# Kernel optimization log

Measured on AMD Instinct MI355X. Metric: run time of the kernel, lower is better.

Reference implementation:

```python
import jax, jax.numpy as jnp
import numpy as np

N = 10000      # atoms
E = 100000     # edges
C = 64         # hidden channels
S = 16         # spherical harmonic components (l_max=3)
NB = 8         # Bessel basis size
HID = 64       # radial MLP hidden
NE = 10        # chemical elements
G = 64         # graphs in batch
L = 2          # interaction layers
HEADS = 1
RC = 5.0       # radial cutoff
AVG_NEI = 16.0


def _sph_l3(u):
    # real spherical harmonics up to l=3, component normalization, on unit vectors u [E,3]
    x, y, z = u[..., 0], u[..., 1], u[..., 2]
    s3 = 3.0 ** 0.5; s5 = 5.0 ** 0.5; s15 = 15.0 ** 0.5
    c1 = (35.0 / 8.0) ** 0.5; c2 = 105.0 ** 0.5; c3 = (21.0 / 8.0) ** 0.5
    c4 = (7.0 / 4.0) ** 0.5; c5 = (105.0 / 4.0) ** 0.5
    comps = [jnp.ones_like(x),
             s3 * x, s3 * y, s3 * z,
             s15 * x * y, s15 * y * z, (s5 / 2) * (3 * z * z - 1), s15 * x * z, (s15 / 2) * (x * x - y * y),
             c1 * y * (3 * x * x - y * y), c2 * x * y * z, c3 * y * (5 * z * z - 1), c4 * z * (5 * z * z - 3),
             c3 * x * (5 * z * z - 1), c5 * z * (x * x - y * y), c1 * x * (x * x - 3 * y * y)]
    return jnp.stack(comps, axis=-1)  # [E, 16]


def _radial(r):
    # Bessel radial basis * polynomial cutoff (p=6); r [E,1] -> [E, NB]
    n = jnp.arange(1, NB + 1, dtype=r.dtype)
    bessel = (2.0 / RC) ** 0.5 * jnp.sin(n * jnp.pi * r / RC) / r
    t = r / RC
    p = 6.0
    fcut = 1.0 - (p + 1) * (p + 2) / 2 * t ** p + p * (p + 2) * t ** (p + 1) - p * (p + 1) / 2 * t ** (p + 2)
    fcut = jnp.where(r < RC, fcut, 0.0)
    return bessel * fcut


def setup_inputs() -> dict:
    key = jax.random.key(0)
    ks = jax.random.split(key, 20)
    positions = jax.random.uniform(ks[0], (N, 3), dtype=jnp.float32) * 6.0
    species = jax.random.randint(ks[1], (N,), 0, NE)
    node_attrs = jax.nn.one_hot(species, NE, dtype=jnp.float32)
    sender = jax.random.randint(ks[2], (E,), 0, N)
    offs = jax.random.randint(ks[3], (E,), 1, N)
    receiver = (sender + offs) % N  # no self loops
    edge_index = jnp.stack([sender, receiver]).astype(jnp.int32)
    batch = jnp.sort(jax.random.randint(ks[4], (N,), 0, G)).astype(jnp.int32)
    head = jnp.zeros((G,), jnp.int32)
    shifts = jnp.zeros((E, 3), jnp.float32)
    ptr = jnp.arange(G + 1, dtype=jnp.int32)
    w = 0.1
    return {
        'positions': positions, 'node_attrs': node_attrs, 'shifts': shifts,
        'atomic_energies': jax.random.normal(ks[5], (HEADS, NE), jnp.float32),
        'W_emb': w * jax.random.normal(ks[6], (NE, C), jnp.float32),
        'W_up': w * jax.random.normal(ks[7], (L, C, C), jnp.float32),
        'mlp_w1': w * jax.random.normal(ks[8], (L, NB, HID), jnp.float32),
        'mlp_w2': w * jax.random.normal(ks[9], (L, HID, HID), jnp.float32),
        'mlp_w3': w * jax.random.normal(ks[10], (L, HID, C * S), jnp.float32),
        'W_mix': w * jax.random.normal(ks[11], (L, C, C), jnp.float32),
        'W_skip': w * jax.random.normal(ks[12], (L, C, NE, C), jnp.float32),
        'Wc': w * jax.random.normal(ks[13], (L, NE, 3, C), jnp.float32),
        'W_out': w * jax.random.normal(ks[14], (L, C, C), jnp.float32),
        'W_ro': w * jax.random.normal(ks[15], (L, C, HEADS), jnp.float32),
        'edge_index': edge_index, 'batch': batch, 'head': head, 'ptr': ptr,
    }


def reference(positions, node_attrs, shifts, atomic_energies, W_emb, W_up, mlp_w1,
              mlp_w2, mlp_w3, W_mix, W_skip, Wc, W_out, W_ro,
              edge_index, batch, head, ptr):
    n_nodes = positions.shape[0]
    n_graphs = ptr.shape[0] - 1
    sender, receiver = edge_index[0], edge_index[1]
    na = jnp.arange(n_nodes)
    node_heads = head[batch]                                   # [N]
    # isolated-atom reference energies
    node_e0 = (node_attrs @ atomic_energies.T)[na, node_heads]  # [N]
    e0 = jax.ops.segment_sum(node_e0, batch, num_segments=n_graphs)
    node_feats = node_attrs @ W_emb                            # [N, C]
    # edge geometry: gather positions by edge index
    vectors = positions[receiver] - positions[sender] + shifts  # [E, 3]
    lengths = jnp.sqrt(jnp.sum(vectors ** 2, axis=-1, keepdims=True))  # [E, 1]
    edge_attrs = _sph_l3(vectors / lengths)                    # [E, S]
    edge_feats = _radial(lengths)                              # [E, NB]
    energies = [e0, jnp.zeros_like(e0)]  # e0, pair_energy (no pair_repulsion)
    for l in range(W_up.shape[0]):
        # radial MLP -> per-edge tensor-product weights
        h = jax.nn.silu(edge_feats @ mlp_w1[l])
        h = jax.nn.silu(h @ mlp_w2[l])
        tp_w = (h @ mlp_w3[l]).reshape(-1, C, S)               # [E, C, S]
        up = node_feats @ W_up[l]                              # [N, C]
        # gather-compute-scatter message passing
        msg = up[sender][:, :, None] * edge_attrs[:, None, :] * tp_w  # [E, C, S]
        A = jax.ops.segment_sum(msg, receiver, num_segments=n_nodes) / AVG_NEI
        A = jnp.einsum('ncs,cd->nds', A, W_mix[l])             # [N, C, S]
        # element-conditioned skip connection
        sc = jnp.einsum('nc,ced,ne->nd', node_feats, W_skip[l], node_attrs)
        # symmetric-contraction product basis (correlation up to 3), element-conditioned
        w = jnp.einsum('ne,ekc->nkc', node_attrs, Wc[l])       # [N, 3, C]
        p1 = A[:, :, 0]
        p2 = jnp.einsum('ncs,ncs->nc', A, A)
        p3 = p2 * p1
        node_feats = (w[:, 0] * p1 + w[:, 1] * p2 + w[:, 2] * p3) @ W_out[l] + sc
        node_en = (node_feats @ W_ro[l])[na, node_heads]       # [N]
        energies.append(jax.ops.segment_sum(node_en, batch, num_segments=n_graphs))
    contributions = jnp.stack(energies, axis=-1)               # [G, L+2]
    return jnp.sum(contributions, axis=-1)                     # [G]
```

## Files before the change

### kernel.cpp

```cpp
#include <hip/hip_runtime.h>

typedef unsigned short u16;
typedef unsigned int u32;
typedef __attribute__((ext_vector_type(8))) short short8;
typedef __attribute__((ext_vector_type(4))) float f32x4;

#define N_NODES 10000
#define N_EDGES 100000
#define C_CH 64
#define S_SPH 16
#define NB_R 8
#define HID_D 64
#define NE_EL 10
#define G_GR 64
#define L_LAY 2
#define N_HEADS 1
#define RCUT 5.0f
#define INV_AVG (1.0f/16.0f)

__device__ __forceinline__ u16 f2bf(float f) {
  u32 u = __float_as_uint(f);
  u32 r = (u + 0x7FFFu + ((u >> 16) & 1u)) >> 16;
  return (u16)r;
}

__global__ void k_init0(float* __restrict__ out, int* __restrict__ deg) {
  int i = blockIdx.x * 256 + threadIdx.x;
  if (i < G_GR) out[i] = 0.0f;
  if (i < N_NODES) deg[i] = 0;
}

__global__ void k_node_init(const float* __restrict__ attrs, const float* __restrict__ ae,
                            const int* __restrict__ batch, const int* __restrict__ head,
                            int* __restrict__ species, float* __restrict__ out) {
  int n = blockIdx.x * 256 + threadIdx.x;
  if (n >= N_NODES) return;
  int sp = 0;
#pragma unroll
  for (int e = 0; e < NE_EL; ++e)
    if (attrs[n * NE_EL + e] > 0.5f) sp = e;
  species[n] = sp;
  int b = batch[n];
  int h = head[b];
  atomicAdd(&out[b], ae[h * NE_EL + sp]);
}

__global__ void k_embed(const int* __restrict__ species, const float* __restrict__ Wemb,
                        float* __restrict__ feats) {
  int idx = blockIdx.x * 256 + threadIdx.x;
  if (idx >= N_NODES * C_CH) return;
  feats[idx] = Wemb[species[idx >> 6] * C_CH + (idx & 63)];
}

__global__ void k_hist(const int* __restrict__ ei, int* __restrict__ deg) {
  int e = blockIdx.x * 256 + threadIdx.x;
  if (e >= N_EDGES) return;
  atomicAdd(&deg[ei[N_EDGES + e]], 1);
}

__global__ void __launch_bounds__(1024) k_scan(const int* __restrict__ deg,
                                               int* __restrict__ rowptr,
                                               int* __restrict__ woff) {
  __shared__ int wsum[16];
  __shared__ int carry_s;
  int tid = threadIdx.x;
  int lane = tid & 63, w = tid >> 6;
  if (tid == 0) carry_s = 0;
  __syncthreads();
  for (int base = 0; base < N_NODES; base += 1024) {
    int i = base + tid;
    int v = (i < N_NODES) ? deg[i] : 0;
    int orig = v;
#pragma unroll
    for (int off = 1; off < 64; off <<= 1) {
      int n = __shfl_up(v, off, 64);
      if (lane >= off) v += n;
    }
    if (lane == 63) wsum[w] = v;
    __syncthreads();
    if (w == 0 && lane < 16) {
      int x = wsum[lane];
#pragma unroll
      for (int off = 1; off < 16; off <<= 1) {
        int n = __shfl_up(x, off, 16);
        if (lane >= off) x += n;
      }
      wsum[lane] = x;
    }
    __syncthreads();
    int waveoff = (w > 0) ? wsum[w - 1] : 0;
    int carry = carry_s;
    int excl = carry + waveoff + v - orig;
    if (i < N_NODES) {
      rowptr[i] = excl;
      woff[i] = excl;
    }
    int tot = wsum[15];
    __syncthreads();
    if (tid == 0) carry_s = carry + tot;
    __syncthreads();
  }
  if (tid == 0) rowptr[N_NODES] = carry_s;
}

__global__ void k_permute(const int* __restrict__ ei, int* __restrict__ woff,
                          int* __restrict__ rank, int* __restrict__ sndp) {
  int e = blockIdx.x * 256 + threadIdx.x;
  if (e >= N_EDGES) return;
  int rdst = ei[N_EDGES + e];
  int pos = atomicAdd(&woff[rdst], 1);
  rank[e] = pos;
  sndp[pos] = ei[e];
}

__global__ void k_geom(const float* __restrict__ pos, const float* __restrict__ shifts,
                       const int* __restrict__ ei, const int* __restrict__ rank,
                       float* __restrict__ Yp, float* __restrict__ radp) {
  int e = blockIdx.x * 256 + threadIdx.x;
  if (e >= N_EDGES) return;
  int s = ei[e], r = ei[N_EDGES + e];
  float dx = pos[r * 3 + 0] - pos[s * 3 + 0] + shifts[e * 3 + 0];
  float dy = pos[r * 3 + 1] - pos[s * 3 + 1] + shifts[e * 3 + 1];
  float dz = pos[r * 3 + 2] - pos[s * 3 + 2] + shifts[e * 3 + 2];
  float rr = sqrtf(dx * dx + dy * dy + dz * dz);
  rr = fmaxf(rr, 1e-12f);
  float inv = 1.0f / rr;
  float x = dx * inv, y = dy * inv, z = dz * inv;
  float xx = x * x, yy = y * y, zz = z * z;
  const float s3 = 1.73205080757f, s5 = 2.2360679775f, s15 = 3.87298334621f;
  const float c1 = 2.09165006634f, c2 = 10.2469507659f, c3 = 1.62018517461f;
  const float c4 = 1.32287565553f, c5 = 5.12347538298f;
  int rk = rank[e];
  float4* Yo = (float4*)(Yp + (size_t)rk * 16);
  Yo[0] = make_float4(1.0f, s3 * x, s3 * y, s3 * z);
  Yo[1] = make_float4(s15 * x * y, s15 * y * z, 0.5f * s5 * (3.0f * zz - 1.0f), s15 * x * z);
  Yo[2] = make_float4(0.5f * s15 * (xx - yy), c1 * y * (3.0f * xx - yy), c2 * x * y * z,
                      c3 * y * (5.0f * zz - 1.0f));
  Yo[3] = make_float4(c4 * z * (5.0f * zz - 3.0f), c3 * x * (5.0f * zz - 1.0f),
                      c5 * z * (xx - yy), c1 * x * (xx - 3.0f * yy));
  float t = rr * (1.0f / RCUT);
  float t2 = t * t;
  float t6 = t2 * t2 * t2;
  float fcut = 1.0f - 28.0f * t6 + 48.0f * t6 * t - 21.0f * t6 * t2;
  if (rr >= RCUT) fcut = 0.0f;
  float pref = 0.63245553203f * inv * fcut;
  float arg = 3.14159265359f * rr * (1.0f / RCUT);
  float sa, ca;
  __sincosf(arg, &sa, &ca);
  float twoc = 2.0f * ca;
  float sprev = 0.0f, scur = sa;
  float rv[8];
#pragma unroll
  for (int n = 0; n < 8; ++n) {
    rv[n] = pref * scur;
    float snext = twoc * scur - sprev;
    sprev = scur;
    scur = snext;
  }
  float4* Ro = (float4*)(radp + (size_t)rk * 8);
  Ro[0] = make_float4(rv[0], rv[1], rv[2], rv[3]);
  Ro[1] = make_float4(rv[4], rv[5], rv[6], rv[7]);
}

__global__ void k_prep(const float* __restrict__ w3, const float* __restrict__ w2,
                       const float* __restrict__ wmix, u16* __restrict__ w3t,
                       u16* __restrict__ w2t, u16* __restrict__ wmixf) {
  int idx = blockIdx.x * 256 + threadIdx.x;
  if (idx < L_LAY * 65536) {
    int l = idx >> 16;
    int r = idx & 65535;
    int k = r & 63;
    int c = (r >> 6) & 63;
    int s = r >> 12;
    w3t[idx] = f2bf(w3[(l * 64 + k) * 1024 + c * 16 + s]);
  } else if (idx < L_LAY * 65536 + L_LAY * 4096) {
    int i = idx - L_LAY * 65536;
    int l = i >> 12;
    int r = i & 4095;
    int t = r >> 6;
    int j = r & 63;
    w2t[l * 4096 + t * 64 + j] = f2bf(w2[(l * 64 + j) * 64 + t]);
  } else if (idx < L_LAY * 65536 + 2 * L_LAY * 4096) {
    int i = idx - L_LAY * 65536 - L_LAY * 4096;
    int l = i >> 12;
    int r = i & 4095;
    int j = r & 7;
    int col = (r >> 3) & 15;
    int kg = (r >> 7) & 3;
    int hf = (r >> 9) & 1;
    int dc = (r >> 10) & 3;
    int c = hf * 32 + kg * 8 + j;
    int d = dc * 16 + col;
    wmixf[l * 4096 + r] = f2bf(wmix[(l * 64 + c) * 64 + d]);
  }
}

__global__ void __launch_bounds__(64) k_edge_mlp(const float* __restrict__ radp,
                                                 const float* __restrict__ w1,
                                                 const u16* __restrict__ w2T,
                                                 u16* __restrict__ h2) {
  __shared__ float w1s[NB_R * HID_D];
  __shared__ __align__(16) u16 h1b[16 * 64];
  int lane = threadIdx.x;
  for (int i = lane; i < NB_R * HID_D; i += 64) w1s[i] = w1[i];
  int er = lane & 15, jg = lane >> 4;
  int eb = blockIdx.x * 16;
  int e = eb + er;
  float4 ra = *(const float4*)(radp + (size_t)e * 8);
  float4 rb = *(const float4*)(radp + (size_t)e * 8 + 4);
  float rv[8] = {ra.x, ra.y, ra.z, ra.w, rb.x, rb.y, rb.z, rb.w};
  u32* hb = (u32*)h1b;
#pragma unroll
  for (int jj = 0; jj < 16; jj += 2) {
    float p0 = 0.f, p1 = 0.f;
#pragma unroll
    for (int k = 0; k < 8; ++k) {
      p0 += rv[k] * w1s[k * 64 + jg * 16 + jj];
      p1 += rv[k] * w1s[k * 64 + jg * 16 + jj + 1];
    }
    p0 = p0 / (1.f + __expf(-p0));
    p1 = p1 / (1.f + __expf(-p1));
    u32 packed = (u32)f2bf(p0) | ((u32)f2bf(p1) << 16);
    int d = jg * 8 + (jj >> 1);
    hb[er * 32 + (d ^ ((er & 7) << 2))] = packed;
  }
  int row = er, kg = jg, col = er;
  const u32* hbr = (const u32*)h1b;
  short8 a0 = *(const short8*)&hbr[row * 32 + ((kg * 4) ^ ((row & 7) << 2))];
  short8 a1 = *(const short8*)&hbr[row * 32 + ((16 + kg * 4) ^ ((row & 7) << 2))];
#pragma unroll
  for (int ch = 0; ch < 4; ++ch) {
    const u16* wp = w2T + (ch * 16 + col) * 64 + kg * 8;
    short8 b0 = *(const short8*)wp;
    short8 b1 = *(const short8*)(wp + 32);
    f32x4 acc = {0.f, 0.f, 0.f, 0.f};
    acc = __builtin_amdgcn_mfma_f32_16x16x32_bf16(a0, b0, acc, 0, 0, 0);
    acc = __builtin_amdgcn_mfma_f32_16x16x32_bf16(a1, b1, acc, 0, 0, 0);
#pragma unroll
    for (int rr = 0; rr < 4; ++rr) {
      float v = acc[rr];
      v = v / (1.f + __expf(-v));
      h2[(size_t)(eb + kg * 4 + rr) * 64 + ch * 16 + col] = f2bf(v);
    }
  }
}

__global__ void __launch_bounds__(256) k_up(const float* __restrict__ feats,
                                            const float* __restrict__ Wup,
                                            float* __restrict__ up) {
  __shared__ float ws[C_CH * C_CH];
  __shared__ float fs[4][C_CH];
  int tid = threadIdx.x;
  for (int i = tid; i < C_CH * C_CH; i += 256) ws[i] = Wup[i];
  __syncthreads();
  int slot = tid >> 6, t = tid & 63;
  for (int nb = blockIdx.x * 4; nb < N_NODES; nb += gridDim.x * 4) {
    int n = nb + slot;
    fs[slot][t] = feats[n * C_CH + t];
    float acc = 0.0f;
#pragma unroll
    for (int j = 0; j < C_CH; ++j) acc += fs[slot][j] * ws[j * C_CH + t];
    up[n * C_CH + t] = acc * INV_AVG;
  }
}

__global__ void __launch_bounds__(256) k_upe(const float* __restrict__ up,
                                             const int* __restrict__ sndp,
                                             float* __restrict__ upe) {
  int tid = threadIdx.x;
  int slot = tid >> 6, t = tid & 63;
  for (int pb = blockIdx.x * 4; pb < N_EDGES; pb += gridDim.x * 4) {
    int pos = pb + slot;
    upe[(size_t)pos * 64 + t] = up[(size_t)sndp[pos] * 64 + t];
  }
}

__global__ void __launch_bounds__(256) k_gather_fused(
    const u16* __restrict__ h2, const u16* __restrict__ W3T, const float* __restrict__ upe,
    const float* __restrict__ Yp, const int* __restrict__ rowptr,
    const u16* __restrict__ WmixF, const float* __restrict__ featsOld,
    float* __restrict__ featsNew, const float* __restrict__ Wskip,
    const float* __restrict__ Wc, const float* __restrict__ WoutG,
    const float* __restrict__ Wro, const int* __restrict__ species,
    const int* __restrict__ batch, const int* __restrict__ headArr,
    float* __restrict__ out) {
  __shared__ __align__(16) float Yt[4][16][20];
  __shared__ __align__(16) u16 Asub[4][16][72];
  __shared__ float qs[4][64];
  __shared__ float fsub[4][64];
  int tid = threadIdx.x;
  int wv = tid >> 6, lane = tid & 63;
  int row = lane & 15, kg = lane >> 4;
  int col = row;
  int cg = wv;
  int cgc = cg * 16 + col;
  int nb = blockIdx.x * 4;
  fsub[wv][lane] = featsOld[(size_t)(nb + wv) * 64 + lane];
  int rp0 = rowptr[nb], rp1 = rowptr[nb + 1], rp2 = rowptr[nb + 2], rp3 = rowptr[nb + 3],
      rp4 = rowptr[nb + 4];
  int d0 = rp1 - rp0, d1 = rp2 - rp1, d2 = rp3 - rp2, d3 = rp4 - rp3;
  int rmax = max(max((d0 + 3) >> 2, (d1 + 3) >> 2), max((d2 + 3) >> 2, (d3 + 3) >> 2));
  rmax = max(rmax, 1);
  int nr = row >> 2;
  int baseA = nr == 0 ? rp0 : nr == 1 ? rp1 : nr == 2 ? rp2 : rp3;
  int degA = nr == 0 ? d0 : nr == 1 ? d1 : nr == 2 ? d2 : d3;
  int baseR = kg == 0 ? rp0 : kg == 1 ? rp1 : kg == 2 ? rp2 : rp3;
  int degR = kg == 0 ? d0 : kg == 1 ? d1 : kg == 2 ? d2 : d3;
  const short8 z8 = {0, 0, 0, 0, 0, 0, 0, 0};

#define LOADR(RR, A0, A1, YQ, U0, U1, U2, U3)                         \
  {                                                                   \
    int sl_ = (RR) * 4 + (row & 3);                                   \
    if (sl_ < degA) {                                                 \
      int eA_ = baseA + sl_;                                          \
      A0 = *(const short8*)(h2 + (size_t)eA_ * 64 + kg * 8);          \
      A1 = *(const short8*)(h2 + (size_t)eA_ * 64 + 32 + kg * 8);     \
      YQ = *(const float4*)(Yp + (size_t)eA_ * 16 + kg * 4);          \
    }                                                                 \
    int s0_ = (RR) * 4;                                               \
    int bb_ = baseR + s0_;                                            \
    U0 = (s0_ + 0 < degR) ? upe[(size_t)(bb_ + 0) * 64 + cgc] : 0.f;  \
    U1 = (s0_ + 1 < degR) ? upe[(size_t)(bb_ + 1) * 64 + cgc] : 0.f;  \
    U2 = (s0_ + 2 < degR) ? upe[(size_t)(bb_ + 2) * 64 + cgc] : 0.f;  \
    U3 = (s0_ + 3 < degR) ? upe[(size_t)(bb_ + 3) * 64 + cgc] : 0.f;  \
  }

#pragma unroll 1
  for (int hf = 0; hf < 2; ++hf) {
    short8 B0[8], B1[8];
#pragma unroll
    for (int ss = 0; ss < 8; ++ss) {
      int s = hf * 8 + ss;
      const u16* wp = W3T + (((s * 64 + cg * 16 + col) << 6) + kg * 8);
      B0[ss] = *(const short8*)wp;
      B1[ss] = *(const short8*)(wp + 32);
    }
    float Areg[8];
#pragma unroll
    for (int ss = 0; ss < 8; ++ss) Areg[ss] = 0.f;
    short8 ca0 = z8, ca1 = z8;
    float4 cyq = make_float4(0.f, 0.f, 0.f, 0.f);
    float cu0, cu1, cu2, cu3;
    LOADR(0, ca0, ca1, cyq, cu0, cu1, cu2, cu3);
#pragma unroll 1
    for (int r = 0; r < rmax; ++r) {
      short8 na0 = z8, na1 = z8;
      float4 nyq = make_float4(0.f, 0.f, 0.f, 0.f);
      float nu0 = 0.f, nu1 = 0.f, nu2 = 0.f, nu3 = 0.f;
      if (r + 1 < rmax) LOADR(r + 1, na0, na1, nyq, nu0, nu1, nu2, nu3);
      Yt[wv][kg * 4 + 0][row] = cyq.x;
      Yt[wv][kg * 4 + 1][row] = cyq.y;
      Yt[wv][kg * 4 + 2][row] = cyq.z;
      Yt[wv][kg * 4 + 3][row] = cyq.w;
#pragma unroll
      for (int ss = 0; ss < 8; ++ss) {
        f32x4 acc = {0.f, 0.f, 0.f, 0.f};
        acc = __builtin_amdgcn_mfma_f32_16x16x32_bf16(ca0, B0[ss], acc, 0, 0, 0);
        acc = __builtin_amdgcn_mfma_f32_16x16x32_bf16(ca1, B1[ss], acc, 0, 0, 0);
        float4 yv = *(const float4*)&Yt[wv][hf * 8 + ss][kg * 4];
        Areg[ss] += acc[0] * yv.x * cu0 + acc[1] * yv.y * cu1 + acc[2] * yv.z * cu2 +
                    acc[3] * yv.w * cu3;
      }
      ca0 = na0;
      ca1 = na1;
      cyq = nyq;
      cu0 = nu0;
      cu1 = nu1;
      cu2 = nu2;
      cu3 = nu3;
    }
#pragma unroll
    for (int ss = 0; ss < 8; ++ss) Asub[kg][hf * 8 + ss][cg * 16 + col] = f2bf(Areg[ss]);
  }
  __syncthreads();

  int sp = species[nb + wv];
  short8 a0m = *(const short8*)&Asub[wv][row][kg * 8];
  short8 a1m = *(const short8*)&Asub[wv][row][32 + kg * 8];
#pragma unroll
  for (int dc = 0; dc < 4; ++dc) {
    short8 wf0 = *(const short8*)(WmixF + (size_t)(dc * 1024 + 0 * 512 + kg * 128 + row * 8));
    short8 wf1 = *(const short8*)(WmixF + (size_t)(dc * 1024 + 1 * 512 + kg * 128 + row * 8));
    f32x4 acc = {0.f, 0.f, 0.f, 0.f};
    acc = __builtin_amdgcn_mfma_f32_16x16x32_bf16(a0m, wf0, acc, 0, 0, 0);
    acc = __builtin_amdgcn_mfma_f32_16x16x32_bf16(a1m, wf1, acc, 0, 0, 0);
    float psq = acc[0] * acc[0] + acc[1] * acc[1] + acc[2] * acc[2] + acc[3] * acc[3];
    psq += __shfl_xor(psq, 16, 64);
    psq += __shfl_xor(psq, 32, 64);
    float p1 = __shfl(acc[0], lane & 15, 64);
    float p3 = psq * p1;
    int d = dc * 16 + row;
    float qv = Wc[(sp * 3 + 0) * 64 + d] * p1 + Wc[(sp * 3 + 1) * 64 + d] * psq +
               Wc[(sp * 3 + 2) * 64 + d] * p3;
    if (kg == 0) qs[wv][d] = qv;
  }

  int t = lane;
  float sc = 0.f;
#pragma unroll 8
  for (int c = 0; c < 64; ++c) sc += fsub[wv][c] * Wskip[(c * NE_EL + sp) * 64 + t];
  float v = sc;
#pragma unroll 8
  for (int d = 0; d < 64; ++d) v += qs[wv][d] * WoutG[d * 64 + t];
  featsNew[(size_t)(nb + wv) * 64 + t] = v;
  int b = batch[nb + wv];
  float en = v * Wro[t * N_HEADS + headArr[b]];
#pragma unroll
  for (int off = 32; off; off >>= 1) en += __shfl_down(en, off, 64);
  if (lane == 0) atomicAdd(&out[b], en);
#undef LOADR
}

extern "C" void kernel_launch(void* const* d_in, const int* in_sizes, int n_in,
                              void* d_out, int out_size, void* d_ws, size_t ws_size,
                              hipStream_t stream) {
  const float* pos = (const float*)d_in[0];
  const float* attrs = (const float*)d_in[1];
  const float* shifts = (const float*)d_in[2];
  const float* ae = (const float*)d_in[3];
  const float* Wemb = (const float*)d_in[4];
  const float* Wup = (const float*)d_in[5];
  const float* w1 = (const float*)d_in[6];
  const float* w2 = (const float*)d_in[7];
  const float* w3 = (const float*)d_in[8];
  const float* Wmix = (const float*)d_in[9];
  const float* Wskip = (const float*)d_in[10];
  const float* Wc = (const float*)d_in[11];
  const float* Wout = (const float*)d_in[12];
  const float* Wro = (const float*)d_in[13];
  const int* ei = (const int*)d_in[14];
  const int* batch = (const int*)d_in[15];
  const int* head = (const int*)d_in[16];
  float* out = (float*)d_out;

  char* p = (char*)d_ws;
  float* Yp = (float*)p;     p += (size_t)N_EDGES * 16 * 4;
  float* radp = (float*)p;   p += (size_t)N_EDGES * 8 * 4;
  float* up = (float*)p;     p += (size_t)N_NODES * 64 * 4;
  float* upe = (float*)p;    p += (size_t)N_EDGES * 64 * 4;
  float* fA = (float*)p;     p += (size_t)N_NODES * 64 * 4;
  float* fB = (float*)p;     p += (size_t)N_NODES * 64 * 4;
  u16* h2 = (u16*)p;         p += (size_t)N_EDGES * 64 * 2;
  u16* W3T = (u16*)p;        p += (size_t)L_LAY * 65536 * 2;
  u16* w2T = (u16*)p;        p += (size_t)L_LAY * 4096 * 2;
  u16* WmixF = (u16*)p;      p += (size_t)L_LAY * 4096 * 2;
  int* species = (int*)p;    p += (size_t)N_NODES * 4;
  int* deg = (int*)p;        p += (size_t)N_NODES * 4;
  int* rowptr = (int*)p;     p += (size_t)(N_NODES + 4) * 4;
  int* woff = (int*)p;       p += (size_t)N_NODES * 4;
  int* rank = (int*)p;       p += (size_t)N_EDGES * 4;
  int* sndp = (int*)p;       p += (size_t)N_EDGES * 4;
  if ((size_t)(p - (char*)d_ws) > ws_size) return;

  k_init0<<<(N_NODES + 255) / 256, 256, 0, stream>>>(out, deg);
  k_node_init<<<(N_NODES + 255) / 256, 256, 0, stream>>>(attrs, ae, batch, head, species, out);
  k_embed<<<(N_NODES * C_CH + 255) / 256, 256, 0, stream>>>(species, Wemb, fA);
  k_hist<<<(N_EDGES + 255) / 256, 256, 0, stream>>>(ei, deg);
  k_scan<<<1, 1024, 0, stream>>>(deg, rowptr, woff);
  k_permute<<<(N_EDGES + 255) / 256, 256, 0, stream>>>(ei, woff, rank, sndp);
  k_geom<<<(N_EDGES + 255) / 256, 256, 0, stream>>>(pos, shifts, ei, rank, Yp, radp);
  k_prep<<<(L_LAY * 65536 + 2 * L_LAY * 4096 + 255) / 256, 256, 0, stream>>>(w3, w2, Wmix, W3T,
                                                                             w2T, WmixF);

  const float* fOld = fA;
  float* fNew = fB;
  for (int l = 0; l < L_LAY; ++l) {
    k_edge_mlp<<<N_EDGES / 16, 64, 0, stream>>>(radp, w1 + l * NB_R * HID_D, w2T + l * 4096, h2);
    k_up<<<512, 256, 0, stream>>>(fOld, Wup + l * C_CH * C_CH, up);
    k_upe<<<2048, 256, 0, stream>>>(up, sndp, upe);
    k_gather_fused<<<N_NODES / 4, 256, 0, stream>>>(
        h2, W3T + l * 65536, upe, Yp, rowptr, WmixF + l * 4096, fOld, fNew,
        Wskip + l * C_CH * NE_EL * C_CH, Wc + l * NE_EL * 3 * C_CH, Wout + l * C_CH * C_CH,
        Wro + l * C_CH * N_HEADS, species, batch, head, out);
    const float* tmp = fNew;
    fNew = (float*)fOld;
    fOld = tmp;
  }
}
```

Before: 461.5 us.

## Stage per-node edge h2 and Y tiles in shared memory for the fused gather

```diff
diff --git a/kernel.cpp b/kernel.cpp
--- a/kernel.cpp
+++ b/kernel.cpp
@@ -163,8 +163,9 @@
 }
 
 __global__ void k_prep(const float* __restrict__ w3, const float* __restrict__ w2,
-                       const float* __restrict__ wmix, u16* __restrict__ w3t,
-                       u16* __restrict__ w2t, u16* __restrict__ wmixf) {
+                       const float* __restrict__ wmix, const float* __restrict__ wskip,
+                       u16* __restrict__ w3t, u16* __restrict__ w2t, u16* __restrict__ wmixf,
+                       float* __restrict__ wskt) {
   int idx = blockIdx.x * 256 + threadIdx.x;
   if (idx < L_LAY * 65536) {
     int l = idx >> 16;
@@ -192,6 +193,16 @@
     int c = hf * 32 + kg * 8 + j;
     int d = dc * 16 + col;
     wmixf[l * 4096 + r] = f2bf(wmix[(l * 64 + c) * 64 + d]);
+  } else if (idx < L_LAY * 65536 + 2 * L_LAY * 4096 + L_LAY * 40960) {
+    int i = idx - (L_LAY * 65536 + 2 * L_LAY * 4096);
+    int l = (i >= 40960) ? 1 : 0;
+    int r = i - l * 40960;
+    int e = r >> 12;
+    int rem = r & 4095;
+    int c = rem >> 6;
+    int d = rem & 63;
+    wskt[(size_t)l * 40960 + e * 4096 + c * 64 + d] =
+        wskip[(size_t)l * 40960 + c * 640 + e * 64 + d];
   }
 }
 
@@ -279,15 +290,17 @@
     const u16* __restrict__ h2, const u16* __restrict__ W3T, const float* __restrict__ upe,
     const float* __restrict__ Yp, const int* __restrict__ rowptr,
     const u16* __restrict__ WmixF, const float* __restrict__ featsOld,
-    float* __restrict__ featsNew, const float* __restrict__ Wskip,
+    float* __restrict__ featsNew, const float* __restrict__ WskT,
     const float* __restrict__ Wc, const float* __restrict__ WoutG,
     const float* __restrict__ Wro, const int* __restrict__ species,
     const int* __restrict__ batch, const int* __restrict__ headArr,
     float* __restrict__ out) {
-  __shared__ __align__(16) float Yt[4][16][20];
+  __shared__ __align__(16) u16 h2s[128 * 64];
+  __shared__ __align__(16) float Yts[16][128];
   __shared__ __align__(16) u16 Asub[4][16][72];
   __shared__ float qs[4][64];
   __shared__ float fsub[4][64];
+  __shared__ int rps[5];
   int tid = threadIdx.x;
   int wv = tid >> 6, lane = tid & 63;
   int row = lane & 15, kg = lane >> 4;
@@ -295,83 +308,92 @@
   int cg = wv;
   int cgc = cg * 16 + col;
   int nb = blockIdx.x * 4;
+  if (tid < 5) rps[tid] = rowptr[nb + tid];
   fsub[wv][lane] = featsOld[(size_t)(nb + wv) * 64 + lane];
-  int rp0 = rowptr[nb], rp1 = rowptr[nb + 1], rp2 = rowptr[nb + 2], rp3 = rowptr[nb + 3],
-      rp4 = rowptr[nb + 4];
+  __syncthreads();
+  int rp0 = rps[0], rp1 = rps[1], rp2 = rps[2], rp3 = rps[3], rp4 = rps[4];
   int d0 = rp1 - rp0, d1 = rp2 - rp1, d2 = rp3 - rp2, d3 = rp4 - rp3;
   int rmax = max(max((d0 + 3) >> 2, (d1 + 3) >> 2), max((d2 + 3) >> 2, (d3 + 3) >> 2));
   rmax = max(rmax, 1);
-  int nr = row >> 2;
-  int baseA = nr == 0 ? rp0 : nr == 1 ? rp1 : nr == 2 ? rp2 : rp3;
-  int degA = nr == 0 ? d0 : nr == 1 ? d1 : nr == 2 ? d2 : d3;
   int baseR = kg == 0 ? rp0 : kg == 1 ? rp1 : kg == 2 ? rp2 : rp3;
   int degR = kg == 0 ? d0 : kg == 1 ? d1 : kg == 2 ? d2 : d3;
-  const short8 z8 = {0, 0, 0, 0, 0, 0, 0, 0};
-
-#define LOADR(RR, A0, A1, YQ, U0, U1, U2, U3)                         \
-  {                                                                   \
-    int sl_ = (RR) * 4 + (row & 3);                                   \
-    if (sl_ < degA) {                                                 \
-      int eA_ = baseA + sl_;                                          \
-      A0 = *(const short8*)(h2 + (size_t)eA_ * 64 + kg * 8);          \
-      A1 = *(const short8*)(h2 + (size_t)eA_ * 64 + 32 + kg * 8);     \
-      YQ = *(const float4*)(Yp + (size_t)eA_ * 16 + kg * 4);          \
-    }                                                                 \
-    int s0_ = (RR) * 4;                                               \
-    int bb_ = baseR + s0_;                                            \
-    U0 = (s0_ + 0 < degR) ? upe[(size_t)(bb_ + 0) * 64 + cgc] : 0.f;  \
-    U1 = (s0_ + 1 < degR) ? upe[(size_t)(bb_ + 1) * 64 + cgc] : 0.f;  \
-    U2 = (s0_ + 2 < degR) ? upe[(size_t)(bb_ + 2) * 64 + cgc] : 0.f;  \
-    U3 = (s0_ + 3 < degR) ? upe[(size_t)(bb_ + 3) * 64 + cgc] : 0.f;  \
-  }
+
+  float Areg[2][8];
+#pragma unroll
+  for (int hf = 0; hf < 2; ++hf)
+#pragma unroll
+    for (int ss = 0; ss < 8; ++ss) Areg[hf][ss] = 0.f;
+
+  const u32* h2sr = (const u32*)h2s;
 
 #pragma unroll 1
-  for (int hf = 0; hf < 2; ++hf) {
-    short8 B0[8], B1[8];
-#pragma unroll
-    for (int ss = 0; ss < 8; ++ss) {
-      int s = hf * 8 + ss;
-      const u16* wp = W3T + (((s * 64 + cg * 16 + col) << 6) + kg * 8);
-      B0[ss] = *(const short8*)wp;
-      B1[ss] = *(const short8*)(wp + 32);
-    }
-    float Areg[8];
-#pragma unroll
-    for (int ss = 0; ss < 8; ++ss) Areg[ss] = 0.f;
-    short8 ca0 = z8, ca1 = z8;
-    float4 cyq = make_float4(0.f, 0.f, 0.f, 0.f);
-    float cu0, cu1, cu2, cu3;
-    LOADR(0, ca0, ca1, cyq, cu0, cu1, cu2, cu3);
+  for (int r0 = 0; r0 < rmax; r0 += 8) {
+    int CH = min(8, rmax - r0);
+    int shift = (CH > 4) ? 5 : 4;
+    int nrows = 4 << shift;
+    __syncthreads();
+    for (int j = tid; j < nrows * 8; j += 256) {
+      int rrow = j >> 3, part = j & 7;
+      int node = rrow >> shift;
+      int sl = r0 * 4 + (rrow & ((1 << shift) - 1));
+      int e = min(rps[node] + sl, N_EDGES - 1);
+      short8 v = *(const short8*)(h2 + (size_t)e * 64 + part * 8);
+      int dsw = (part * 4) ^ (((rrow ^ (rrow >> 3)) & 7) << 2);
+      *(short8*)((u32*)h2s + rrow * 32 + dsw) = v;
+    }
+    for (int j = tid; j < nrows * 4; j += 256) {
+      int rrow = j >> 2, part = j & 3;
+      int node = rrow >> shift;
+      int sl = r0 * 4 + (rrow & ((1 << shift) - 1));
+      int e = min(rps[node] + sl, N_EDGES - 1);
+      float4 y = *(const float4*)(Yp + (size_t)e * 16 + part * 4);
+      Yts[part * 4 + 0][rrow] = y.x;
+      Yts[part * 4 + 1][rrow] = y.y;
+      Yts[part * 4 + 2][rrow] = y.z;
+      Yts[part * 4 + 3][rrow] = y.w;
+    }
+    __syncthreads();
 #pragma unroll 1
-    for (int r = 0; r < rmax; ++r) {
-      short8 na0 = z8, na1 = z8;
-      float4 nyq = make_float4(0.f, 0.f, 0.f, 0.f);
-      float nu0 = 0.f, nu1 = 0.f, nu2 = 0.f, nu3 = 0.f;
-      if (r + 1 < rmax) LOADR(r + 1, na0, na1, nyq, nu0, nu1, nu2, nu3);
-      Yt[wv][kg * 4 + 0][row] = cyq.x;
-      Yt[wv][kg * 4 + 1][row] = cyq.y;
-      Yt[wv][kg * 4 + 2][row] = cyq.z;
-      Yt[wv][kg * 4 + 3][row] = cyq.w;
+    for (int hf = 0; hf < 2; ++hf) {
+      short8 B0[8], B1[8];
 #pragma unroll
       for (int ss = 0; ss < 8; ++ss) {
-        f32x4 acc = {0.f, 0.f, 0.f, 0.f};
-        acc = __builtin_amdgcn_mfma_f32_16x16x32_bf16(ca0, B0[ss], acc, 0, 0, 0);
-        acc = __builtin_amdgcn_mfma_f32_16x16x32_bf16(ca1, B1[ss], acc, 0, 0, 0);
-        float4 yv = *(const float4*)&Yt[wv][hf * 8 + ss][kg * 4];
-        Areg[ss] += acc[0] * yv.x * cu0 + acc[1] * yv.y * cu1 + acc[2] * yv.z * cu2 +
-                    acc[3] * yv.w * cu3;
+        int s = hf * 8 + ss;
+        const u16* wp = W3T + (((s * 64 + cg * 16 + col) << 6) + kg * 8);
+        B0[ss] = *(const short8*)wp;
+        B1[ss] = *(const short8*)(wp + 32);
       }
-      ca0 = na0;
-      ca1 = na1;
-      cyq = nyq;
-      cu0 = nu0;
-      cu1 = nu1;
-      cu2 = nu2;
-      cu3 = nu3;
-    }
-#pragma unroll
-    for (int ss = 0; ss < 8; ++ss) Asub[kg][hf * 8 + ss][cg * 16 + col] = f2bf(Areg[ss]);
-  }
+#pragma unroll 1
+      for (int rl = 0; rl < CH; ++rl) {
+        int srow = ((row >> 2) << shift) + rl * 4 + (row & 3);
+        int swz = (((srow ^ (srow >> 3)) & 7) << 2);
+        short8 a0 = *(const short8*)(h2sr + srow * 32 + ((kg * 4) ^ swz));
+        short8 a1 = *(const short8*)(h2sr + srow * 32 + ((16 + kg * 4) ^ swz));
+        int slq = (r0 + rl) * 4;
+        float upv[4];
+#pragma unroll
+        for (int q = 0; q < 4; ++q) {
+          int pos = min(baseR + slq + q, N_EDGES - 1);
+          float u = upe[(size_t)pos * 64 + cgc];
+          upv[q] = (slq + q < degR) ? u : 0.f;
+        }
+        int ybase = (kg << shift) + rl * 4;
+#pragma unroll
+        for (int ss = 0; ss < 8; ++ss) {
+          f32x4 acc = {0.f, 0.f, 0.f, 0.f};
+          acc = __builtin_amdgcn_mfma_f32_16x16x32_bf16(a0, B0[ss], acc, 0, 0, 0);
+          acc = __builtin_amdgcn_mfma_f32_16x16x32_bf16(a1, B1[ss], acc, 0, 0, 0);
+          float4 yv = *(const float4*)&Yts[hf * 8 + ss][ybase];
+          Areg[hf][ss] += acc[0] * yv.x * upv[0] + acc[1] * yv.y * upv[1] +
+                          acc[2] * yv.z * upv[2] + acc[3] * yv.w * upv[3];
+        }
+      }
+    }
+  }
+#pragma unroll
+  for (int hf = 0; hf < 2; ++hf)
+#pragma unroll
+    for (int ss = 0; ss < 8; ++ss) Asub[kg][hf * 8 + ss][cg * 16 + col] = f2bf(Areg[hf][ss]);
   __syncthreads();
 
   int sp = species[nb + wv];
@@ -396,9 +418,10 @@
   }
 
   int t = lane;
+  const float* wsk = WskT + (size_t)sp * 4096;
   float sc = 0.f;
 #pragma unroll 8
-  for (int c = 0; c < 64; ++c) sc += fsub[wv][c] * Wskip[(c * NE_EL + sp) * 64 + t];
+  for (int c = 0; c < 64; ++c) sc += fsub[wv][c] * wsk[c * 64 + t];
   float v = sc;
 #pragma unroll 8
   for (int d = 0; d < 64; ++d) v += qs[wv][d] * WoutG[d * 64 + t];
@@ -408,7 +431,6 @@
 #pragma unroll
   for (int off = 32; off; off >>= 1) en += __shfl_down(en, off, 64);
   if (lane == 0) atomicAdd(&out[b], en);
-#undef LOADR
 }
 
 extern "C" void kernel_launch(void* const* d_in, const int* in_sizes, int n_in,
@@ -444,6 +466,7 @@
   u16* W3T = (u16*)p;        p += (size_t)L_LAY * 65536 * 2;
   u16* w2T = (u16*)p;        p += (size_t)L_LAY * 4096 * 2;
   u16* WmixF = (u16*)p;      p += (size_t)L_LAY * 4096 * 2;
+  float* WskT = (float*)p;   p += (size_t)L_LAY * 40960 * 4;
   int* species = (int*)p;    p += (size_t)N_NODES * 4;
   int* deg = (int*)p;        p += (size_t)N_NODES * 4;
   int* rowptr = (int*)p;     p += (size_t)(N_NODES + 4) * 4;
@@ -459,8 +482,8 @@
   k_scan<<<1, 1024, 0, stream>>>(deg, rowptr, woff);
   k_permute<<<(N_EDGES + 255) / 256, 256, 0, stream>>>(ei, woff, rank, sndp);
   k_geom<<<(N_EDGES + 255) / 256, 256, 0, stream>>>(pos, shifts, ei, rank, Yp, radp);
-  k_prep<<<(L_LAY * 65536 + 2 * L_LAY * 4096 + 255) / 256, 256, 0, stream>>>(w3, w2, Wmix, W3T,
-                                                                             w2T, WmixF);
+  int prepTot = L_LAY * 65536 + 2 * L_LAY * 4096 + L_LAY * 40960;
+  k_prep<<<(prepTot + 255) / 256, 256, 0, stream>>>(w3, w2, Wmix, Wskip, W3T, w2T, WmixF, WskT);
 
   const float* fOld = fA;
   float* fNew = fB;
@@ -470,7 +493,7 @@
     k_upe<<<2048, 256, 0, stream>>>(up, sndp, upe);
     k_gather_fused<<<N_NODES / 4, 256, 0, stream>>>(
         h2, W3T + l * 65536, upe, Yp, rowptr, WmixF + l * 4096, fOld, fNew,
-        Wskip + l * C_CH * NE_EL * C_CH, Wc + l * NE_EL * 3 * C_CH, Wout + l * C_CH * C_CH,
+        WskT + (size_t)l * 40960, Wc + l * NE_EL * 3 * C_CH, Wout + l * C_CH * C_CH,
         Wro + l * C_CH * N_HEADS, species, batch, head, out);
     const float* tmp = fNew;
     fNew = (float*)fOld;
```

Result: faster. 452.0 us (-2.0%).
